# Optimization experiments

Measured on AMD Instinct MI355X. Metric: run time of the kernel, lower is better.

## Reference

```python
import jax, jax.numpy as jnp
import numpy as np


def swiglu(g, u):
    return jax.nn.silu(g) * u


def setup_inputs() -> dict:
    key = jax.random.key(0)
    ks = jax.random.split(key, 10)
    D, H, E, HS = 2048, 512, 32, 1024
    B, S = 1, 2048
    s = 0.02
    return {
        "x": jax.random.normal(ks[0], (B, S, D), jnp.float32),
        "gate_w": jax.random.normal(ks[1], (E, D), jnp.float32) * s,
        "expert_bias": jnp.zeros((E,), jnp.float32),
        "wg": jax.random.normal(ks[2], (E, D, H), jnp.float32) * s,
        "wu": jax.random.normal(ks[3], (E, D, H), jnp.float32) * s,
        "wd": jax.random.normal(ks[4], (E, H, D), jnp.float32) * s,
        "sg": jax.random.normal(ks[5], (D, HS), jnp.float32) * s,
        "su": jax.random.normal(ks[6], (D, HS), jnp.float32) * s,
        "sd": jax.random.normal(ks[7], (HS, D), jnp.float32) * s,
        "coef_w": jax.random.normal(ks[8], (2, D), jnp.float32) * s,
        "coef_b": jnp.zeros((2,), jnp.float32),
        "top_k": 4,
    }


def reference(x, gate_w, expert_bias, wg, wu, wd, sg, su, sd, coef_w, coef_b, top_k):
    # --- sigmoid router with bias-adjusted top-k selection ---
    logits = jnp.einsum("bsd,ed->bse", x, gate_w)            # [B,S,E]
    routing = jax.nn.sigmoid(logits.astype(jnp.float32))
    biased = routing + expert_bias[None, None, :]
    _, inds = jax.lax.top_k(biased, top_k)                    # [B,S,k]
    scores = jnp.take_along_axis(routing, inds, axis=-1)      # gather UNbiased weights
    scores = scores / (jnp.sum(scores, axis=-1, keepdims=True) + 1e-20)  # norm_topk_prob
    scores = scores.astype(x.dtype)

    # --- SwitchGLU experts: dense per-expert SwiGLU, then gather top-k outputs ---
    h = jnp.einsum("bsd,edh->bseh", x, wg)                    # [B,S,E,H]
    u = jnp.einsum("bsd,edh->bseh", x, wu)
    y_all = jnp.einsum("bseh,ehd->bsed", swiglu(h, u), wd)    # [B,S,E,D]
    expert_out = jnp.take_along_axis(
        y_all, inds[..., None], axis=2)                        # [B,S,k,D]
    y_experts = jnp.sum(expert_out * scores[..., None], axis=-2)  # [B,S,D]

    # --- shared expert + learned 2-way mixing coefficient ---
    shared = swiglu(x @ sg, x @ su) @ sd                      # [B,S,D]
    coef = jax.nn.softmax(jnp.einsum("bsd,cd->bsc", x, coef_w) + coef_b, axis=-1)
    return y_experts * coef[..., :1] + shared * coef[..., 1:]
```

## Files before the change

kernel.cpp:

```cpp
#include <hip/hip_runtime.h>
#include <hip/hip_bf16.h>
#include <stdint.h>

#define S_TOK   2048
#define DMODEL  2048
#define HEXP    512
#define NEXP    32
#define HSH     1024
#define NPAIR   (S_TOK * 4)
#define NT128   96

#define M128_NT  0
#define M128_TE  1
#define M128_TP0 (1 + NT128)
#define M128_TM  (1 + 2 * NT128)
#define META_SIZE (1 + 3 * NT128)

typedef short  s16x8 __attribute__((ext_vector_type(8)));
typedef __bf16 b16x8 __attribute__((ext_vector_type(8)));
typedef float  f32x4 __attribute__((ext_vector_type(4)));

__device__ __forceinline__ f32x4 mfma16x16x32(s16x8 a, s16x8 b, f32x4 c) {
    return __builtin_amdgcn_mfma_f32_16x16x32_bf16(
        __builtin_bit_cast(b16x8, a), __builtin_bit_cast(b16x8, b), c, 0, 0, 0);
}

__device__ __forceinline__ unsigned short f2bf(float f) {
    union { float f; unsigned int u; } v; v.f = f;
    unsigned int u = v.u;
    return (unsigned short)((u + 0x7FFFu + ((u >> 16) & 1u)) >> 16);
}

__device__ __forceinline__ float bf2f(unsigned short b) {
    union { unsigned int u; float f; } v; v.u = ((unsigned int)b) << 16;
    return v.f;
}

__device__ __forceinline__ void gload16(const unsigned short* g, unsigned short* l) {
    __builtin_amdgcn_global_load_lds(
        (const __attribute__((address_space(1))) void*)(uintptr_t)g,
        (__attribute__((address_space(3))) void*)(uintptr_t)l, 16, 0, 0);
}

__device__ __forceinline__ int src_col8(int lane) {
    return 8 * ((lane & 3) ^ ((lane >> 3) & 3));
}
__device__ __forceinline__ int frag_ko(int fr, int fq) {
    return 8 * (fq ^ ((fr >> 1) & 3));
}

__device__ __forceinline__ void tconv_tile(const float* __restrict__ s,
                                           unsigned short* __restrict__ d,
                                           const int K, const int N,
                                           const int k0, const int n0,
                                           unsigned short* pool)
{
    auto T = (unsigned short (*)[84])pool;
    const int tid = threadIdx.x;
    const int n4 = (tid & 15) * 4;
    const int kr = tid >> 4;
#pragma unroll
    for (int i = 0; i < 4; ++i) {
        const int k = kr + i * 16;
        const float4 v = *reinterpret_cast<const float4*>(s + (size_t)(k0 + k) * N + n0 + n4);
        T[n4 + 0][k] = f2bf(v.x);
        T[n4 + 1][k] = f2bf(v.y);
        T[n4 + 2][k] = f2bf(v.z);
        T[n4 + 3][k] = f2bf(v.w);
    }
    __syncthreads();
    const int nw = tid >> 2;
    const int kc = (tid & 3) * 16;
    unsigned short* o = d + (size_t)(n0 + nw) * K + k0 + kc;
#pragma unroll
    for (int j = 0; j < 4; ++j)
        *reinterpret_cast<uint2*>(o + j * 4) =
            *reinterpret_cast<const uint2*>(&T[nw][kc + j * 4]);
}

__global__ __launch_bounds__(256)
void router_kernel(const float* __restrict__ x, const float* __restrict__ gate_w,
                   const float* __restrict__ expert_bias,
                   const float* __restrict__ coef_w, const float* __restrict__ coef_b,
                   int* __restrict__ inds, float* __restrict__ scores,
                   float* __restrict__ coefo)
{
    const int t = blockIdx.x;
    const int tid = threadIdx.x;
    const int lane = tid & 63;
    const int wave = tid >> 6;
    const float* xr = x + (size_t)t * DMODEL;

    float xv[32];
#pragma unroll
    for (int j = 0; j < 32; ++j) xv[j] = xr[lane + 64 * j];

    __shared__ float s_logits[NEXP];
    __shared__ float s_coef[2];

    for (int i = 0; i < 8; ++i) {
        const int e = wave * 8 + i;
        const float* wr = gate_w + (size_t)e * DMODEL;
        float p = 0.f;
#pragma unroll
        for (int j = 0; j < 32; ++j) p += xv[j] * wr[lane + 64 * j];
#pragma unroll
        for (int o = 32; o > 0; o >>= 1) p += __shfl_xor(p, o);
        if (lane == 0) s_logits[e] = p;
    }
    if (wave == 0) {
        for (int c = 0; c < 2; ++c) {
            const float* wr = coef_w + (size_t)c * DMODEL;
            float p = 0.f;
#pragma unroll
            for (int j = 0; j < 32; ++j) p += xv[j] * wr[lane + 64 * j];
#pragma unroll
            for (int o = 32; o > 0; o >>= 1) p += __shfl_xor(p, o);
            if (lane == 0) s_coef[c] = p;
        }
    }
    __syncthreads();
    if (tid == 0) {
        float routing[NEXP], biased[NEXP];
        for (int e = 0; e < NEXP; ++e) {
            const float r = 1.f / (1.f + expf(-s_logits[e]));
            routing[e] = r;
            biased[e] = r + expert_bias[e];
        }
        int sel[4]; float sc[4]; float ssum = 0.f;
        for (int k = 0; k < 4; ++k) {
            int best = 0; float bv = -1e30f;
            for (int e = 0; e < NEXP; ++e)
                if (biased[e] > bv) { bv = biased[e]; best = e; }
            sel[k] = best; sc[k] = routing[best]; ssum += sc[k];
            biased[best] = -1e30f;
        }
        const float inv = 1.f / (ssum + 1e-20f);
        for (int k = 0; k < 4; ++k) {
            inds[t * 4 + k] = sel[k];
            scores[t * 4 + k] = sc[k] * inv;
        }
        const float l0 = s_coef[0] + coef_b[0];
        const float l1 = s_coef[1] + coef_b[1];
        const float m = fmaxf(l0, l1);
        const float e0 = expf(l0 - m), e1 = expf(l1 - m);
        coefo[t * 2 + 0] = e0 / (e0 + e1);
        coefo[t * 2 + 1] = e1 / (e0 + e1);
    }
}

__global__ __launch_bounds__(256)
void xcast_kernel(const float* __restrict__ x, unsigned short* __restrict__ xb)
{
    const int i = (blockIdx.x * 256 + threadIdx.x) * 4;
    const float4 v = *reinterpret_cast<const float4*>(x + i);
    ushort4 o;
    o.x = f2bf(v.x); o.y = f2bf(v.y); o.z = f2bf(v.z); o.w = f2bf(v.w);
    *reinterpret_cast<ushort4*>(xb + i) = o;
}

__global__ __launch_bounds__(256)
void tconv_all_kernel(const float* __restrict__ wg, const float* __restrict__ wu,
                      const float* __restrict__ sg, const float* __restrict__ su,
                      const float* __restrict__ sd,
                      unsigned short* __restrict__ W1, unsigned short* __restrict__ W2,
                      unsigned short* __restrict__ sgb, unsigned short* __restrict__ sub_,
                      unsigned short* __restrict__ sdb)
{
    __shared__ unsigned short pool[64 * 84];
    const int bid = blockIdx.x;
    if (bid < 8192) {
        const int e = bid >> 8, t = bid & 255;
        tconv_tile(wg + (size_t)e * DMODEL * HEXP, W1 + (size_t)e * HEXP * DMODEL,
                   DMODEL, HEXP, ((t >> 3) & 31) * 64, (t & 7) * 64, pool);
    } else if (bid < 16384) {
        const int e = (bid - 8192) >> 8, t = bid & 255;
        tconv_tile(wu + (size_t)e * DMODEL * HEXP, W2 + (size_t)e * HEXP * DMODEL,
                   DMODEL, HEXP, ((t >> 3) & 31) * 64, (t & 7) * 64, pool);
    } else if (bid < 16896) {
        const int t = bid - 16384;
        tconv_tile(sg, sgb, DMODEL, HSH, (t >> 4) * 64, (t & 15) * 64, pool);
    } else if (bid < 17408) {
        const int t = bid - 16896;
        tconv_tile(su, sub_, DMODEL, HSH, (t >> 4) * 64, (t & 15) * 64, pool);
    } else {
        const int t = bid - 17408;
        tconv_tile(sd, sdb, HSH, DMODEL, (t >> 5) * 64, (t & 31) * 64, pool);
    }
}

__global__ __launch_bounds__(256)
void tconv_wd_kernel(const float* __restrict__ wd, unsigned short* __restrict__ wdb)
{
    __shared__ unsigned short pool[64 * 84];
    const int e = blockIdx.x >> 8, t = blockIdx.x & 255;
    tconv_tile(wd + (size_t)e * HEXP * DMODEL, wdb + (size_t)e * DMODEL * HEXP,
               HEXP, DMODEL, (t >> 5) * 64, (t & 31) * 64, pool);
}

__global__ __launch_bounds__(1024)
void group_kernel(const int* __restrict__ inds, const float* __restrict__ scores,
                  int* __restrict__ meta, int* __restrict__ pair_token,
                  float* __restrict__ pair_score, int* __restrict__ tok_pos)
{
    __shared__ int cnt[NEXP];
    __shared__ int off_s[NEXP];
    __shared__ int cur[NEXP];
    const int tid = threadIdx.x;
    if (tid < NEXP) cnt[tid] = 0;
    __syncthreads();
    for (int i = tid; i < NPAIR; i += 1024) atomicAdd(&cnt[inds[i]], 1);
    __syncthreads();
    if (tid == 0) {
        int run = 0, nt1 = 0;
        for (int e = 0; e < NEXP; ++e) {
            off_s[e] = run;
            const int c = cnt[e];
            for (int m0 = 0; m0 < c; m0 += 128) {
                meta[M128_TE + nt1] = e;
                meta[M128_TP0 + nt1] = run + m0;
                meta[M128_TM + nt1] = (c - m0 < 128) ? (c - m0) : 128;
                ++nt1;
            }
            run += c;
        }
        meta[M128_NT] = nt1;
    }
    __syncthreads();
    if (tid < NEXP) cur[tid] = off_s[tid];
    __syncthreads();
    for (int i = tid; i < NPAIR; i += 1024) {
        const int e = inds[i];
        const int pos = atomicAdd(&cur[e], 1);
        pair_token[pos] = i >> 2;
        pair_score[pos] = scores[i];
        tok_pos[i] = pos;
    }
}

__global__ __launch_bounds__(256, 3)
void gu128_kernel(const unsigned short* __restrict__ xb,
                  const unsigned short* __restrict__ W1,
                  const unsigned short* __restrict__ W2,
                  const int* __restrict__ meta, const int* __restrict__ pair_token,
                  const unsigned short* __restrict__ sgb,
                  const unsigned short* __restrict__ sub_,
                  unsigned short* __restrict__ hexp, unsigned short* __restrict__ uexp,
                  unsigned short* __restrict__ shh, unsigned short* __restrict__ shu)
{
    constexpr int NT = DMODEL / 32;
    __shared__ unsigned short Al[2][128][32];
    __shared__ unsigned short Bl[2][128][32];

    const int bid = blockIdx.x;
    const int tid = threadIdx.x;
    const int lane = tid & 63;
    const int wave = tid >> 6;
    const int fr = lane & 15, fq = lane >> 4;
    const int ko = frag_ko(fr, fq);
    const int sub = lane >> 2;
    const int col8 = src_col8(lane);
    const int wm = wave >> 1, wn = wave & 1;
    const f32x4 zero4 = {0.f, 0.f, 0.f, 0.f};

    const bool EXPERT = bid < 8 * NT128;
    int p0, mval, n0, NB;
    const unsigned short* B;
    unsigned short* obuf;
    int tok0, tok1;
    const int arow0 = wave * 32 + sub;
    if (EXPERT) {
        const int tt = bid >> 3;
        if (tt >= meta[M128_NT]) return;
        const int e = meta[M128_TE + tt];
        p0 = meta[M128_TP0 + tt];
        mval = meta[M128_TM + tt];
        const int r = bid & 7;
        const int mat = r >> 2;
        n0 = (r & 3) * 128;
        NB = HEXP;
        B = (mat ? W2 : W1) + (size_t)e * HEXP * DMODEL;
        obuf = mat ? uexp : hexp;
        int q0 = p0 + arow0;      if (q0 > NPAIR - 1) q0 = NPAIR - 1;
        int q1 = p0 + arow0 + 16; if (q1 > NPAIR - 1) q1 = NPAIR - 1;
        tok0 = pair_token[q0];
        tok1 = pair_token[q1];
    } else {
        const int idx = bid - 8 * NT128;
        const int mat = idx & 1;
        n0 = ((idx >> 1) & 7) * 128;
        p0 = (idx >> 4) * 128;
        mval = 128;
        NB = HSH;
        B = mat ? sub_ : sgb;
        obuf = mat ? shu : shh;
        tok0 = p0 + arow0;
        tok1 = p0 + arow0 + 16;
    }

    const unsigned short* asrc0 = xb + (size_t)tok0 * DMODEL + col8;
    const unsigned short* asrc1 = xb + (size_t)tok1 * DMODEL + col8;
    const unsigned short* bsrc0 = B + (size_t)(n0 + arow0) * DMODEL + col8;
    const unsigned short* bsrc1 = B + (size_t)(n0 + arow0 + 16) * DMODEL + col8;

    auto stage = [&](int buf, int k0) {
        gload16(asrc0 + k0, &Al[buf][wave * 32][0]);
        gload16(asrc1 + k0, &Al[buf][wave * 32 + 16][0]);
        gload16(bsrc0 + k0, &Bl[buf][wave * 32][0]);
        gload16(bsrc1 + k0, &Bl[buf][wave * 32 + 16][0]);
    };

    f32x4 acc[4][4];
#pragma unroll
    for (int m = 0; m < 4; ++m)
#pragma unroll
        for (int n = 0; n < 4; ++n) acc[m][n] = zero4;

    auto compute = [&](int buf) {
        s16x8 af[4], bf[4];
#pragma unroll
        for (int m = 0; m < 4; ++m)
            af[m] = *reinterpret_cast<const s16x8*>(&Al[buf][wm * 64 + m * 16 + fr][ko]);
#pragma unroll
        for (int n = 0; n < 4; ++n)
            bf[n] = *reinterpret_cast<const s16x8*>(&Bl[buf][wn * 64 + n * 16 + fr][ko]);
#pragma unroll
        for (int m = 0; m < 4; ++m)
#pragma unroll
            for (int n = 0; n < 4; ++n)
                acc[m][n] = mfma16x16x32(af[m], bf[n], acc[m][n]);
    };

    stage(0, 0);
    __syncthreads();
#pragma unroll 1
    for (int t = 0; t < NT; ++t) {
        const int cur = t & 1;
        if (t + 1 < NT) stage(cur ^ 1, (t + 1) * 32);
        compute(cur);
        __syncthreads();
    }

#pragma unroll
    for (int m = 0; m < 4; ++m)
#pragma unroll
        for (int n = 0; n < 4; ++n) {
            const int col = n0 + wn * 64 + n * 16 + fr;
#pragma unroll
            for (int r = 0; r < 4; ++r) {
                const int rt = wm * 64 + m * 16 + fq * 4 + r;
                if (rt < mval)
                    obuf[(size_t)(p0 + rt) * NB + col] = f2bf(acc[m][n][r]);
            }
        }
}

__global__ __launch_bounds__(256)
void swiglu_kernel(const unsigned short* __restrict__ hexp,
                   const unsigned short* __restrict__ uexp,
                   unsigned short* __restrict__ act,
                   const unsigned short* __restrict__ shh,
                   const unsigned short* __restrict__ shu,
                   unsigned short* __restrict__ shact)
{
    constexpr size_t NE = (size_t)NPAIR * HEXP;
    const size_t i = ((size_t)blockIdx.x * 256 + threadIdx.x) * 8;
    const unsigned short *hp, *up;
    unsigned short* ap;
    size_t j;
    if (i < NE) { hp = hexp; up = uexp; ap = act; j = i; }
    else        { hp = shh;  up = shu;  ap = shact; j = i - NE; }
    const uint4 hv = *reinterpret_cast<const uint4*>(hp + j);
    const uint4 uv = *reinterpret_cast<const uint4*>(up + j);
    const unsigned short* hu = reinterpret_cast<const unsigned short*>(&hv);
    const unsigned short* uu = reinterpret_cast<const unsigned short*>(&uv);
    ushort4 o[2];
    unsigned short* ou = reinterpret_cast<unsigned short*>(o);
#pragma unroll
    for (int k = 0; k < 8; ++k) {
        const float h = bf2f(hu[k]);
        const float u = bf2f(uu[k]);
        ou[k] = f2bf(h / (1.f + __expf(-h)) * u);
    }
    *reinterpret_cast<uint4*>(ap + j) = *reinterpret_cast<const uint4*>(o);
}

__global__ __launch_bounds__(256, 3)
void down128_kernel(const unsigned short* __restrict__ act,
                    const unsigned short* __restrict__ shact,
                    const unsigned short* __restrict__ wdb,
                    const unsigned short* __restrict__ sdb,
                    unsigned short* __restrict__ ypair,
                    float* __restrict__ sdown,
                    const int* __restrict__ meta,
                    const float* __restrict__ pair_score)
{
    __shared__ unsigned short Al[2][128][32];
    __shared__ unsigned short Bl[2][128][32];

    const int bid = blockIdx.x;
    const int tid = threadIdx.x;
    const int lane = tid & 63;
    const int wave = tid >> 6;
    const int fr = lane & 15, fq = lane >> 4;
    const int ko = frag_ko(fr, fq);
    const int sub = lane >> 2;
    const int col8 = src_col8(lane);
    const int wm = wave >> 1, wn = wave & 1;
    const f32x4 zero4 = {0.f, 0.f, 0.f, 0.f};

    const bool EXPERT = bid < 16 * NT128;
    int p0, mval, n0, KA;
    const unsigned short *Asrc, *B;
    if (EXPERT) {
        const int tt = bid >> 4;
        if (tt >= meta[M128_NT]) return;
        const int e = meta[M128_TE + tt];
        p0 = meta[M128_TP0 + tt];
        mval = meta[M128_TM + tt];
        n0 = (bid & 15) * 128;
        KA = HEXP;
        Asrc = act;
        B = wdb + (size_t)e * DMODEL * HEXP;
    } else {
        const int idx = bid - 16 * NT128;
        p0 = (idx >> 4) * 128;
        mval = 128;
        n0 = (idx & 15) * 128;
        KA = HSH;
        Asrc = shact;
        B = sdb;
    }
    const int NT = KA / 32;

    const int arow0 = wave * 32 + sub;
    const unsigned short* asrc0 = Asrc + (size_t)(p0 + arow0) * KA + col8;
    const unsigned short* asrc1 = Asrc + (size_t)(p0 + arow0 + 16) * KA + col8;
    const unsigned short* bsrc0 = B + (size_t)(n0 + arow0) * KA + col8;
    const unsigned short* bsrc1 = B + (size_t)(n0 + arow0 + 16) * KA + col8;

    auto stage = [&](int buf, int k0) {
        gload16(asrc0 + k0, &Al[buf][wave * 32][0]);
        gload16(asrc1 + k0, &Al[buf][wave * 32 + 16][0]);
        gload16(bsrc0 + k0, &Bl[buf][wave * 32][0]);
        gload16(bsrc1 + k0, &Bl[buf][wave * 32 + 16][0]);
    };

    f32x4 acc[4][4];
#pragma unroll
    for (int m = 0; m < 4; ++m)
#pragma unroll
        for (int n = 0; n < 4; ++n) acc[m][n] = zero4;

    auto compute = [&](int buf) {
        s16x8 af[4], bf[4];
#pragma unroll
        for (int m = 0; m < 4; ++m)
            af[m] = *reinterpret_cast<const s16x8*>(&Al[buf][wm * 64 + m * 16 + fr][ko]);
#pragma unroll
        for (int n = 0; n < 4; ++n)
            bf[n] = *reinterpret_cast<const s16x8*>(&Bl[buf][wn * 64 + n * 16 + fr][ko]);
#pragma unroll
        for (int m = 0; m < 4; ++m)
#pragma unroll
            for (int n = 0; n < 4; ++n)
                acc[m][n] = mfma16x16x32(af[m], bf[n], acc[m][n]);
    };

    stage(0, 0);
    __syncthreads();
#pragma unroll 1
    for (int t = 0; t < NT; ++t) {
        const int cur = t & 1;
        if (t + 1 < NT) stage(cur ^ 1, (t + 1) * 32);
        compute(cur);
        __syncthreads();
    }

#pragma unroll
    for (int m = 0; m < 4; ++m)
#pragma unroll
        for (int n = 0; n < 4; ++n) {
            const int col = n0 + wn * 64 + n * 16 + fr;
#pragma unroll
            for (int r = 0; r < 4; ++r) {
                const int rt = wm * 64 + m * 16 + fq * 4 + r;
                if (rt < mval) {
                    if (EXPERT) {
                        const int p = p0 + rt;
                        ypair[(size_t)p * DMODEL + col] = f2bf(acc[m][n][r] * pair_score[p]);
                    } else {
                        sdown[(size_t)(p0 + rt) * DMODEL + col] = acc[m][n][r];
                    }
                }
            }
        }
}

__global__ __launch_bounds__(256)
void final_kernel(const unsigned short* __restrict__ ypair,
                  const float* __restrict__ sdown,
                  const float* __restrict__ coef, const int* __restrict__ tok_pos,
                  float* __restrict__ out)
{
    const int row = blockIdx.x;
    const int col = threadIdx.x * 8;
    float acc[8] = {0.f, 0.f, 0.f, 0.f, 0.f, 0.f, 0.f, 0.f};
#pragma unroll
    for (int k = 0; k < 4; ++k) {
        const int pos = tok_pos[row * 4 + k];
        const uint4 v = *reinterpret_cast<const uint4*>(ypair + (size_t)pos * DMODEL + col);
        const unsigned short* u = reinterpret_cast<const unsigned short*>(&v);
#pragma unroll
        for (int j = 0; j < 8; ++j) acc[j] += bf2f(u[j]);
    }
    const float c0 = coef[row * 2 + 0];
    const float c1 = coef[row * 2 + 1];
    const float* sd = sdown + (size_t)row * DMODEL + col;
    const float4 s0 = *reinterpret_cast<const float4*>(sd);
    const float4 s1 = *reinterpret_cast<const float4*>(sd + 4);
    float4 o0, o1;
    o0.x = acc[0] * c0 + s0.x * c1; o0.y = acc[1] * c0 + s0.y * c1;
    o0.z = acc[2] * c0 + s0.z * c1; o0.w = acc[3] * c0 + s0.w * c1;
    o1.x = acc[4] * c0 + s1.x * c1; o1.y = acc[5] * c0 + s1.y * c1;
    o1.z = acc[6] * c0 + s1.z * c1; o1.w = acc[7] * c0 + s1.w * c1;
    float* op = out + (size_t)row * DMODEL + col;
    *reinterpret_cast<float4*>(op) = o0;
    *reinterpret_cast<float4*>(op + 4) = o1;
}

extern "C" void kernel_launch(void* const* d_in, const int* in_sizes, int n_in,
                              void* d_out, int out_size, void* d_ws, size_t ws_size,
                              hipStream_t stream)
{
    const float* x           = (const float*)d_in[0];
    const float* gate_w      = (const float*)d_in[1];
    const float* expert_bias = (const float*)d_in[2];
    const float* wg          = (const float*)d_in[3];
    const float* wu          = (const float*)d_in[4];
    const float* wd          = (const float*)d_in[5];
    const float* sg          = (const float*)d_in[6];
    const float* su          = (const float*)d_in[7];
    const float* sd          = (const float*)d_in[8];
    const float* coef_w      = (const float*)d_in[9];
    const float* coef_b      = (const float*)d_in[10];
    float* out = (float*)d_out;

    char* ws = (char*)d_ws;
    size_t off = 0;
    auto take = [&](size_t bytes) {
        char* p = ws + off;
        off = (off + bytes + 255) & ~(size_t)255;
        return p;
    };
    int*   inds     = (int*)  take((size_t)S_TOK * 4 * sizeof(int));
    float* scores   = (float*)take((size_t)S_TOK * 4 * sizeof(float));
    float* coefp    = (float*)take((size_t)S_TOK * 2 * sizeof(float));
    int*   meta     = (int*)  take((size_t)META_SIZE * sizeof(int));
    int*   pair_tok = (int*)  take((size_t)NPAIR * sizeof(int));
    float* pair_sc  = (float*)take((size_t)NPAIR * sizeof(float));
    int*   tok_pos  = (int*)  take((size_t)NPAIR * sizeof(int));
    unsigned short* xb    = (unsigned short*)take((size_t)S_TOK * DMODEL * 2);
    unsigned short* act   = (unsigned short*)take((size_t)NPAIR * HEXP * 2);
    unsigned short* hexp  = (unsigned short*)take((size_t)NPAIR * HEXP * 2);
    unsigned short* uexp  = (unsigned short*)take((size_t)NPAIR * HEXP * 2);
    unsigned short* shact = (unsigned short*)take((size_t)S_TOK * HSH * 2);
    unsigned short* shh   = (unsigned short*)take((size_t)S_TOK * HSH * 2);
    unsigned short* shu   = (unsigned short*)take((size_t)S_TOK * HSH * 2);
    unsigned short* ypair = (unsigned short*)take((size_t)NPAIR * DMODEL * 2);
    float*          sdown = (float*)take((size_t)S_TOK * DMODEL * 4);
    unsigned short* sgb   = (unsigned short*)take((size_t)HSH * DMODEL * 2);
    unsigned short* sub_  = (unsigned short*)take((size_t)HSH * DMODEL * 2);
    unsigned short* sdb   = (unsigned short*)take((size_t)DMODEL * HSH * 2);
    unsigned short* W1    = (unsigned short*)take((size_t)NEXP * DMODEL * HEXP * 2);
    unsigned short* W2    = (unsigned short*)take((size_t)NEXP * DMODEL * HEXP * 2);
    (void)ws_size; (void)in_sizes; (void)n_in; (void)out_size;

    router_kernel<<<S_TOK, 256, 0, stream>>>(x, gate_w, expert_bias, coef_w, coef_b,
                                             inds, scores, coefp);
    xcast_kernel<<<(S_TOK * DMODEL / 4) / 256, 256, 0, stream>>>(x, xb);
    group_kernel<<<1, 1024, 0, stream>>>(inds, scores, meta, pair_tok, pair_sc, tok_pos);

    tconv_all_kernel<<<17920, 256, 0, stream>>>(wg, wu, sg, su, sd,
                                                W1, W2, sgb, sub_, sdb);

    gu128_kernel<<<8 * NT128 + 256, 256, 0, stream>>>(
        xb, W1, W2, meta, pair_tok, sgb, sub_, hexp, uexp, shh, shu);

    swiglu_kernel<<<3072, 256, 0, stream>>>(hexp, uexp, act, shh, shu, shact);

    tconv_wd_kernel<<<NEXP * 256, 256, 0, stream>>>(wd, W1);

    down128_kernel<<<16 * NT128 + 256, 256, 0, stream>>>(
        act, shact, W1, sdb, ypair, sdown, meta, pair_sc);

    final_kernel<<<S_TOK, 256, 0, stream>>>(ypair, sdown, coefp, tok_pos, out);
}
```

Measured before the change: 348.8 us.

## Overlap wd/sd weight conversion with gate-up GEMM and widen transpose stores

Moves the fp32-to-bf16 transposed conversion of the down-projection weights (wd and sd) out of their own launch and out of tconv_all. They now run as extra blocks appended to the gate/up GEMM grid, so the memory-bound conversion can overlap the compute-bound GEMM and one kernel launch goes away. The converted wd goes into a new buffer instead of reusing W1, which costs extra workspace memory. The transpose tile's stores are also widened from four 8-byte writes to two 16-byte writes. The GEMM's shared memory is now a single pool reused by the conversion blocks.

```diff
diff --git a/kernel.cpp b/kernel.cpp
--- a/kernel.cpp
+++ b/kernel.cpp
@@ -71,11 +71,16 @@
     __syncthreads();
     const int nw = tid >> 2;
     const int kc = (tid & 3) * 16;
+    const uint2 a0 = *reinterpret_cast<const uint2*>(&T[nw][kc]);
+    const uint2 a1 = *reinterpret_cast<const uint2*>(&T[nw][kc + 4]);
+    const uint2 a2 = *reinterpret_cast<const uint2*>(&T[nw][kc + 8]);
+    const uint2 a3 = *reinterpret_cast<const uint2*>(&T[nw][kc + 12]);
+    uint4 w0, w1;
+    w0.x = a0.x; w0.y = a0.y; w0.z = a1.x; w0.w = a1.y;
+    w1.x = a2.x; w1.y = a2.y; w1.z = a3.x; w1.w = a3.y;
     unsigned short* o = d + (size_t)(n0 + nw) * K + k0 + kc;
-#pragma unroll
-    for (int j = 0; j < 4; ++j)
-        *reinterpret_cast<uint2*>(o + j * 4) =
-            *reinterpret_cast<const uint2*>(&T[nw][kc + j * 4]);
+    *reinterpret_cast<uint4*>(o)     = w0;
+    *reinterpret_cast<uint4*>(o + 8) = w1;
 }
 
 __global__ __launch_bounds__(256)
@@ -162,10 +167,8 @@
 __global__ __launch_bounds__(256)
 void tconv_all_kernel(const float* __restrict__ wg, const float* __restrict__ wu,
                       const float* __restrict__ sg, const float* __restrict__ su,
-                      const float* __restrict__ sd,
                       unsigned short* __restrict__ W1, unsigned short* __restrict__ W2,
-                      unsigned short* __restrict__ sgb, unsigned short* __restrict__ sub_,
-                      unsigned short* __restrict__ sdb)
+                      unsigned short* __restrict__ sgb, unsigned short* __restrict__ sub_)
 {
     __shared__ unsigned short pool[64 * 84];
     const int bid = blockIdx.x;
@@ -180,22 +183,10 @@
     } else if (bid < 16896) {
         const int t = bid - 16384;
         tconv_tile(sg, sgb, DMODEL, HSH, (t >> 4) * 64, (t & 15) * 64, pool);
-    } else if (bid < 17408) {
+    } else {
         const int t = bid - 16896;
         tconv_tile(su, sub_, DMODEL, HSH, (t >> 4) * 64, (t & 15) * 64, pool);
-    } else {
-        const int t = bid - 17408;
-        tconv_tile(sd, sdb, HSH, DMODEL, (t >> 5) * 64, (t & 31) * 64, pool);
-    }
-}
-
-__global__ __launch_bounds__(256)
-void tconv_wd_kernel(const float* __restrict__ wd, unsigned short* __restrict__ wdb)
-{
-    __shared__ unsigned short pool[64 * 84];
-    const int e = blockIdx.x >> 8, t = blockIdx.x & 255;
-    tconv_tile(wd + (size_t)e * HEXP * DMODEL, wdb + (size_t)e * DMODEL * HEXP,
-               HEXP, DMODEL, (t >> 5) * 64, (t & 31) * 64, pool);
+    }
 }
 
 __global__ __launch_bounds__(1024)
@@ -246,16 +237,33 @@
                   const unsigned short* __restrict__ sgb,
                   const unsigned short* __restrict__ sub_,
                   unsigned short* __restrict__ hexp, unsigned short* __restrict__ uexp,
-                  unsigned short* __restrict__ shh, unsigned short* __restrict__ shu)
+                  unsigned short* __restrict__ shh, unsigned short* __restrict__ shu,
+                  const float* __restrict__ wd, unsigned short* __restrict__ wdb,
+                  const float* __restrict__ sd, unsigned short* __restrict__ sdb)
 {
     constexpr int NT = DMODEL / 32;
-    __shared__ unsigned short Al[2][128][32];
-    __shared__ unsigned short Bl[2][128][32];
+    __shared__ unsigned short pool[16384];
+    auto Al = (unsigned short (*)[128][32])(pool);
+    auto Bl = (unsigned short (*)[128][32])(pool + 8192);
 
     const int bid = blockIdx.x;
     const int tid = threadIdx.x;
     const int lane = tid & 63;
     const int wave = tid >> 6;
+
+    if (bid >= 8 * NT128 + 256) {
+        const int idx = bid - (8 * NT128 + 256);
+        if (idx < 8192) {
+            const int e = idx >> 8, t = idx & 255;
+            tconv_tile(wd + (size_t)e * HEXP * DMODEL, wdb + (size_t)e * DMODEL * HEXP,
+                       HEXP, DMODEL, (t >> 5) * 64, (t & 31) * 64, pool);
+        } else {
+            const int t = idx - 8192;
+            tconv_tile(sd, sdb, HSH, DMODEL, (t >> 5) * 64, (t & 31) * 64, pool);
+        }
+        return;
+    }
+
     const int fr = lane & 15, fq = lane >> 4;
     const int ko = frag_ko(fr, fq);
     const int sub = lane >> 2;
@@ -574,6 +582,7 @@
     unsigned short* sdb   = (unsigned short*)take((size_t)DMODEL * HSH * 2);
     unsigned short* W1    = (unsigned short*)take((size_t)NEXP * DMODEL * HEXP * 2);
     unsigned short* W2    = (unsigned short*)take((size_t)NEXP * DMODEL * HEXP * 2);
+    unsigned short* wdb   = (unsigned short*)take((size_t)NEXP * DMODEL * HEXP * 2);
     (void)ws_size; (void)in_sizes; (void)n_in; (void)out_size;
 
     router_kernel<<<S_TOK, 256, 0, stream>>>(x, gate_w, expert_bias, coef_w, coef_b,
@@ -581,18 +590,16 @@
     xcast_kernel<<<(S_TOK * DMODEL / 4) / 256, 256, 0, stream>>>(x, xb);
     group_kernel<<<1, 1024, 0, stream>>>(inds, scores, meta, pair_tok, pair_sc, tok_pos);
 
-    tconv_all_kernel<<<17920, 256, 0, stream>>>(wg, wu, sg, su, sd,
-                                                W1, W2, sgb, sub_, sdb);
-
-    gu128_kernel<<<8 * NT128 + 256, 256, 0, stream>>>(
-        xb, W1, W2, meta, pair_tok, sgb, sub_, hexp, uexp, shh, shu);
+    tconv_all_kernel<<<17408, 256, 0, stream>>>(wg, wu, sg, su, W1, W2, sgb, sub_);
+
+    gu128_kernel<<<8 * NT128 + 256 + 8704, 256, 0, stream>>>(
+        xb, W1, W2, meta, pair_tok, sgb, sub_, hexp, uexp, shh, shu,
+        wd, wdb, sd, sdb);
 
     swiglu_kernel<<<3072, 256, 0, stream>>>(hexp, uexp, act, shh, shu, shact);
 
-    tconv_wd_kernel<<<NEXP * 256, 256, 0, stream>>>(wd, W1);
-
     down128_kernel<<<16 * NT128 + 256, 256, 0, stream>>>(
-        act, shact, W1, sdb, ypair, sdown, meta, pair_sc);
+        act, shact, wdb, sdb, ypair, sdown, meta, pair_sc);
 
     final_kernel<<<S_TOK, 256, 0, stream>>>(ypair, sdown, coefp, tok_pos, out);
 }
```

After: 333.6 us. 4.4% less time.
